# Kernel tuning notes

Measured on AMD Instinct MI355X. Metric: run time of the kernel, lower is better.

The kernel has to match this reference:

```python
import jax, jax.numpy as jnp
import numpy as np
import math

BS = 8  # JPEG block size
QUALITY = 250.0  # __scale_quality(20) = 5000/20
OFFSET = 128.0 / 255.0


def _dctmtx(bs=BS):
    m = np.empty((bs, bs), dtype=np.float32)
    for j in range(bs):
        for i in range(bs):
            if i == 0:
                m[i, j] = 1.0 / math.sqrt(bs)
            else:
                m[i, j] = math.sqrt(2.0 / bs) * math.cos(math.pi * (2 * j + 1) * i / (2 * bs))
    return jnp.asarray(m)


XFORM = jnp.array([[0.299, 0.587, 0.114],
                   [-0.168735892, -0.331264108, 0.5],
                   [0.5, -0.418687589, -0.081312411]], dtype=jnp.float32)


def setup_inputs() -> dict:
    key = jax.random.key(0)
    k1, k2 = jax.random.split(key)
    rgb = jax.random.uniform(k1, (16, 3, 512, 512), dtype=jnp.float32)
    # qtable: round(abs(t)+0.5)/255 -> positive integers / 255
    quantize = jax.random.randint(k2, (3, BS, BS), 1, 100).astype(jnp.float32) / 255.0
    return {"rgb": rgb, "quantize": quantize}


def _blockify(x, bs=BS):
    # x: [B, H, W] -> [B, H//bs, W//bs, bs, bs]
    b, h, w = x.shape
    return x.reshape(b, h // bs, bs, w // bs, bs).transpose(0, 1, 3, 2, 4)


def reference(rgb, quantize):
    B, C, H, W = rgb.shape
    dct = _dctmtx()
    # RGB -> YCbCr (BHWC matmul with xform^T, expressed on BCHW via einsum)
    ycbcr = jnp.einsum('bchw,kc->bkhw', rgb, XFORM)
    shift = jnp.array([0.0, OFFSET, OFFSET], dtype=rgb.dtype)[None, :, None, None]
    ycbcr = jnp.clip(ycbcr + shift, 0.0, 1.0) - OFFSET
    # chroma 2x2 mean subsample
    y = ycbcr[:, 0]                                            # [B, H, W]
    cbcr = ycbcr[:, 1:].reshape(B, 2, H // 2, 2, W // 2, 2).mean(axis=(3, 5))
    channels = [y, cbcr[:, 0], cbcr[:, 1]]
    outs = []
    for i, ch in enumerate(channels):
        blocks = _blockify(ch)                                 # [B, nh, nw, 8, 8]
        dcts = jnp.einsum('ij,bhwjk,lk->bhwil', dct, blocks, dct)
        denom = quantize[i] * (QUALITY / 100.0) + 0.5 / 255.0  # [8, 8]
        comp = jnp.round(dcts / denom)
        outs.append(comp.reshape(-1, BS, BS))
    return tuple(outs)
```

## Files before the change

kernel.cpp:

```cpp
#include <hip/hip_runtime.h>
#include <math.h>


static __device__ __forceinline__ float clip01(float v) {
    return fminf(fmaxf(v, 0.0f), 1.0f);
}

#define M1f 0.49039264020161522f
#define M2f 0.46193976625564337f
#define M3f 0.41573480615127262f
#define M4f 0.35355339059327376f
#define M5f 0.27778511650980111f
#define M6f 0.19134171618254489f
#define M7f 0.097545161008064134f

static constexpr float Dm[8][8] = {
    { M4f,  M4f,  M4f,  M4f,  M4f,  M4f,  M4f,  M4f},
    { M1f,  M3f,  M5f,  M7f, -M7f, -M5f, -M3f, -M1f},
    { M2f,  M6f, -M6f, -M2f, -M2f, -M6f,  M6f,  M2f},
    { M3f, -M7f, -M1f, -M5f,  M5f,  M1f,  M7f, -M3f},
    { M4f, -M4f, -M4f,  M4f,  M4f, -M4f, -M4f,  M4f},
    { M5f, -M1f,  M7f,  M3f, -M3f, -M7f,  M1f, -M5f},
    { M6f, -M2f,  M2f, -M6f, -M6f,  M2f, -M2f,  M6f},
    { M7f, -M5f,  M3f, -M1f,  M1f, -M3f,  M5f, -M7f},
};

__global__ __launch_bounds__(256)
void jpeg_kernel(const float* __restrict__ rgb, const float* __restrict__ quant,
                 float* __restrict__ out)
{
    __shared__ __align__(16) float smem[4224];
    constexpr int YT  = 0;
    constexpr int CBF = 1152;
    constexpr int CRF = 2304;
    constexpr int TMP = 1152;
    constexpr int CB8 = 3456;
    constexpr int CR8 = 3744;
    constexpr int QNT = 4032;

    const int t = threadIdx.x;

    if (t < 192) smem[QNT + t] = quant[t];

    const int wg   = blockIdx.x;
    const int b    = wg >> 8;
    const int tile = wg & 255;
    const int th   = tile >> 4;
    const int tw   = tile & 15;

    {
        const int row = t >> 3;
        const int c4  = (t & 7) << 2;
        const float* p = rgb + ((size_t)b * 3) * 262144 + (size_t)(th * 32 + row) * 512 + (tw * 32 + c4);
        const float4 R  = *(const float4*)p;
        const float4 G  = *(const float4*)(p + 262144);
        const float4 Bv = *(const float4*)(p + 524288);
        const float OFF = (float)(128.0 / 255.0);
        const float rr[4] = {R.x, R.y, R.z, R.w};
        const float gg[4] = {G.x, G.y, G.z, G.w};
        const float bb[4] = {Bv.x, Bv.y, Bv.z, Bv.w};
        float yv[4], cbv[4], crv[4];
        #pragma unroll
        for (int k = 0; k < 4; ++k) {
            const float r_ = rr[k], g_ = gg[k], b_ = bb[k];
            const float y  = (float)(0.299) * r_ + (float)(0.587) * g_ + (float)(0.114) * b_;
            const float cb = (float)(-0.168735892) * r_ + (float)(-0.331264108) * g_ + 0.5f * b_;
            const float cr = 0.5f * r_ + (float)(-0.418687589) * g_ + (float)(-0.081312411) * b_;
            yv[k]  = clip01(y) - OFF;
            cbv[k] = clip01(cb + OFF);
            crv[k] = clip01(cr + OFF);
        }
        *(float4*)&smem[YT  + row * 36 + c4] = make_float4(yv[0], yv[1], yv[2], yv[3]);
        *(float4*)&smem[CBF + row * 36 + c4] = make_float4(cbv[0], cbv[1], cbv[2], cbv[3]);
        *(float4*)&smem[CRF + row * 36 + c4] = make_float4(crv[0], crv[1], crv[2], crv[3]);
    }
    __syncthreads();

    {
        const float OFF = (float)(128.0 / 255.0);
        const int pr = t >> 4, pc = t & 15;
        const int o00 = (2 * pr) * 36 + 2 * pc;
        const int o10 = o00 + 36;
        float sb = smem[CBF + o00];
        sb = sb + smem[CBF + o00 + 1];
        sb = sb + smem[CBF + o10];
        sb = sb + smem[CBF + o10 + 1];
        smem[CB8 + pr * 18 + pc] = sb * 0.25f - OFF;
        const float cr_r0 = smem[CRF + o00] + smem[CRF + o00 + 1];
        const float cr_r1 = smem[CRF + o10] + smem[CRF + o10 + 1];
        smem[CR8 + pr * 18 + pc] = (cr_r0 + cr_r1) * 0.25f - OFF;
    }
    __syncthreads();

    const int w  = t >> 6;
    const int l  = t & 63;
    const int bi = l >> 3;
    const int lc = l & 7;

    if (bi < 6) {
        const int sb = w * 6 + bi;
        int xoff, ldx, ch; size_t obase;
        if (sb < 16) {
            const int sr = sb >> 2, sc = sb & 3;
            xoff = YT + sr * 288 + sc * 8; ldx = 36; ch = 0;
            obase = (((size_t)(b * 64 + th * 4 + sr)) * 64 + (tw * 4 + sc)) * 64;
        } else if (sb < 20) {
            const int s = sb - 16, sr = s >> 1, sc = s & 1;
            xoff = CB8 + sr * 144 + sc * 8; ldx = 18; ch = 1;
            obase = (size_t)4194304 + (((size_t)(b * 32 + th * 2 + sr)) * 32 + (tw * 2 + sc)) * 64;
        } else {
            const int s = sb - 20, sr = s >> 1, sc = s & 1;
            xoff = CR8 + sr * 144 + sc * 8; ldx = 18; ch = 2;
            obase = (size_t)5242880 + (((size_t)(b * 32 + th * 2 + sr)) * 32 + (tw * 2 + sc)) * 64;
        }

        float x[8];
        #pragma unroll
        for (int j = 0; j < 8; ++j) x[j] = smem[xoff + j * ldx + lc];
        const int tbase = TMP + w * 408 + bi * 68;
        #pragma unroll
        for (int i = 0; i < 8; ++i) {
            float s = 0.0f;
            #pragma unroll
            for (int j = 0; j < 8; ++j) s += Dm[i][j] * x[j];
            smem[tbase + i * 8 + lc] = s;
        }

        float tr[8], q[8];
        *(float4*)&tr[0] = *(const float4*)&smem[tbase + lc * 8];
        *(float4*)&tr[4] = *(const float4*)&smem[tbase + lc * 8 + 4];
        *(float4*)&q[0]  = *(const float4*)&smem[QNT + ch * 64 + lc * 8];
        *(float4*)&q[4]  = *(const float4*)&smem[QNT + ch * 64 + lc * 8 + 4];

        const float qadd = (float)(0.5 / 255.0);
        float o[8];
        #pragma unroll
        for (int cc = 0; cc < 8; ++cc) {
            float s = 0.0f;
            #pragma unroll
            for (int k = 0; k < 8; ++k) s += tr[k] * Dm[cc][k];
            const float den = __fadd_rn(__fmul_rn(q[cc], 2.5f), qadd);
            o[cc] = rintf(s / den);
        }
        float* op = out + obase + lc * 8;
        *(float4*)&op[0] = make_float4(o[0], o[1], o[2], o[3]);
        *(float4*)&op[4] = make_float4(o[4], o[5], o[6], o[7]);
    }
}

extern "C" void kernel_launch(void* const* d_in, const int* in_sizes, int n_in,
                              void* d_out, int out_size, void* d_ws, size_t ws_size,
                              hipStream_t stream) {
    const float* rgb   = (const float*)d_in[0];
    const float* quant = (const float*)d_in[1];
    float* out = (float*)d_out;
    dim3 grid(4096), block(256);
    hipLaunchKernelGGL(jpeg_kernel, grid, block, 0, stream, rgb, quant, out);
}
```

Before: 18.05 us.

## Fuse chroma subsampling into color conversion and store tiles transposed in LDS

Each thread now loads a 2x2 pixel quad as float2 pairs, so chroma 2x2 averaging happens in registers. This removes the full-resolution Cb/Cr LDS staging, one barrier and the separate subsample pass. Y and the subsampled chroma are written to shared memory transposed, so the column DCT pass can fetch its 8 inputs with two float4 LDS reads instead of eight strided scalar loads. The cost is that global loads become float2 instead of float4, and the transposed scalar and float2 LDS writes may cause bank conflicts.

```diff
diff --git a/kernel.cpp b/kernel.cpp
--- a/kernel.cpp
+++ b/kernel.cpp
@@ -29,14 +29,12 @@
 void jpeg_kernel(const float* __restrict__ rgb, const float* __restrict__ quant,
                  float* __restrict__ out)
 {
-    __shared__ __align__(16) float smem[4224];
-    constexpr int YT  = 0;
-    constexpr int CBF = 1152;
-    constexpr int CRF = 2304;
-    constexpr int TMP = 1152;
-    constexpr int CB8 = 3456;
-    constexpr int CR8 = 3744;
-    constexpr int QNT = 4032;
+    __shared__ __align__(16) float smem[3616];
+    constexpr int YTT = 0;
+    constexpr int CBT = 1152;
+    constexpr int CRT = 1472;
+    constexpr int QNT = 1792;
+    constexpr int TMP = 1984;
 
     const int t = threadIdx.x;
 
@@ -49,16 +47,20 @@
     const int tw   = tile & 15;
 
     {
-        const int row = t >> 3;
-        const int c4  = (t & 7) << 2;
-        const float* p = rgb + ((size_t)b * 3) * 262144 + (size_t)(th * 32 + row) * 512 + (tw * 32 + c4);
-        const float4 R  = *(const float4*)p;
-        const float4 G  = *(const float4*)(p + 262144);
-        const float4 Bv = *(const float4*)(p + 524288);
+        const int qr = t >> 4;
+        const int qc = t & 15;
+        const int r0 = 2 * qr, c0 = 2 * qc;
+        const float* p = rgb + ((size_t)b * 3) * 262144 + (size_t)(th * 32 + r0) * 512 + (tw * 32 + c0);
+        const float2 R0 = *(const float2*)p;
+        const float2 R1 = *(const float2*)(p + 512);
+        const float2 G0 = *(const float2*)(p + 262144);
+        const float2 G1 = *(const float2*)(p + 262144 + 512);
+        const float2 B0 = *(const float2*)(p + 524288);
+        const float2 B1 = *(const float2*)(p + 524288 + 512);
         const float OFF = (float)(128.0 / 255.0);
-        const float rr[4] = {R.x, R.y, R.z, R.w};
-        const float gg[4] = {G.x, G.y, G.z, G.w};
-        const float bb[4] = {Bv.x, Bv.y, Bv.z, Bv.w};
+        const float rr[4] = {R0.x, R0.y, R1.x, R1.y};
+        const float gg[4] = {G0.x, G0.y, G1.x, G1.y};
+        const float bb[4] = {B0.x, B0.y, B1.x, B1.y};
         float yv[4], cbv[4], crv[4];
         #pragma unroll
         for (int k = 0; k < 4; ++k) {
@@ -70,25 +72,18 @@
             cbv[k] = clip01(cb + OFF);
             crv[k] = clip01(cr + OFF);
         }
-        *(float4*)&smem[YT  + row * 36 + c4] = make_float4(yv[0], yv[1], yv[2], yv[3]);
-        *(float4*)&smem[CBF + row * 36 + c4] = make_float4(cbv[0], cbv[1], cbv[2], cbv[3]);
-        *(float4*)&smem[CRF + row * 36 + c4] = make_float4(crv[0], crv[1], crv[2], crv[3]);
-    }
-    __syncthreads();
-
-    {
-        const float OFF = (float)(128.0 / 255.0);
-        const int pr = t >> 4, pc = t & 15;
-        const int o00 = (2 * pr) * 36 + 2 * pc;
-        const int o10 = o00 + 36;
-        float sb = smem[CBF + o00];
-        sb = sb + smem[CBF + o00 + 1];
-        sb = sb + smem[CBF + o10];
-        sb = sb + smem[CBF + o10 + 1];
-        smem[CB8 + pr * 18 + pc] = sb * 0.25f - OFF;
-        const float cr_r0 = smem[CRF + o00] + smem[CRF + o00 + 1];
-        const float cr_r1 = smem[CRF + o10] + smem[CRF + o10 + 1];
-        smem[CR8 + pr * 18 + pc] = (cr_r0 + cr_r1) * 0.25f - OFF;
+        *(float2*)&smem[YTT + c0 * 36 + r0]       = make_float2(yv[0], yv[2]);
+        *(float2*)&smem[YTT + (c0 + 1) * 36 + r0] = make_float2(yv[1], yv[3]);
+        float sb = cbv[0];
+        sb = sb + cbv[1];
+        sb = sb + cbv[2];
+        sb = sb + cbv[3];
+        smem[CBT + qc * 20 + qr] = sb * 0.25f - OFF;
+        float sr = crv[0];
+        sr = sr + crv[1];
+        sr = sr + crv[2];
+        sr = sr + crv[3];
+        smem[CRT + qc * 20 + qr] = sr * 0.25f - OFF;
     }
     __syncthreads();
 
@@ -99,24 +94,24 @@
 
     if (bi < 6) {
         const int sb = w * 6 + bi;
-        int xoff, ldx, ch; size_t obase;
+        int xaddr, ch; size_t obase;
         if (sb < 16) {
             const int sr = sb >> 2, sc = sb & 3;
-            xoff = YT + sr * 288 + sc * 8; ldx = 36; ch = 0;
+            xaddr = YTT + (sc * 8 + lc) * 36 + sr * 8; ch = 0;
             obase = (((size_t)(b * 64 + th * 4 + sr)) * 64 + (tw * 4 + sc)) * 64;
         } else if (sb < 20) {
             const int s = sb - 16, sr = s >> 1, sc = s & 1;
-            xoff = CB8 + sr * 144 + sc * 8; ldx = 18; ch = 1;
+            xaddr = CBT + (sc * 8 + lc) * 20 + sr * 8; ch = 1;
             obase = (size_t)4194304 + (((size_t)(b * 32 + th * 2 + sr)) * 32 + (tw * 2 + sc)) * 64;
         } else {
             const int s = sb - 20, sr = s >> 1, sc = s & 1;
-            xoff = CR8 + sr * 144 + sc * 8; ldx = 18; ch = 2;
+            xaddr = CRT + (sc * 8 + lc) * 20 + sr * 8; ch = 2;
             obase = (size_t)5242880 + (((size_t)(b * 32 + th * 2 + sr)) * 32 + (tw * 2 + sc)) * 64;
         }
 
         float x[8];
-        #pragma unroll
-        for (int j = 0; j < 8; ++j) x[j] = smem[xoff + j * ldx + lc];
+        *(float4*)&x[0] = *(const float4*)&smem[xaddr];
+        *(float4*)&x[4] = *(const float4*)&smem[xaddr + 4];
         const int tbase = TMP + w * 408 + bi * 68;
         #pragma unroll
         for (int i = 0; i < 8; ++i) {
```

Result: no change. 17.97 us (-0.5%).
